# Optimization experiments

Measured on AMD Instinct MI355X. Metric: run time of the kernel, lower is better.

Reference implementation:

```python
import jax, jax.numpy as jnp
import numpy as np

KERNEL_SIZE = 4
SCALE = 0.5


def setup_inputs() -> dict:
    key = jax.random.key(0)
    k1, k2, k3 = jax.random.split(key, 3)
    M, K, N = 16384, 1024, 4096
    x = jax.random.normal(k1, (M, K), dtype=jnp.float32)
    weight = jax.random.normal(k2, (N, K), dtype=jnp.float32)
    bias = jax.random.normal(k3, (N,), dtype=jnp.float32)
    return {"x": x, "weight": weight, "bias": bias}


def reference(x, weight, bias):
    # y = x @ W^T + b : (M, N)
    y = jnp.einsum('mk,nk->mn', x, weight) + bias[None, :]
    M, N = y.shape
    valid_n = (N // KERNEL_SIZE) * KERNEL_SIZE
    # MaxPool1d(kernel_size, stride=kernel_size): (M, N//k, k) -> max over window
    pooled = jnp.max(y[:, :valid_n].reshape(M, valid_n // KERNEL_SIZE, KERNEL_SIZE), axis=-1)
    # sum over pooled features, then scale -> (M,)
    return jnp.sum(pooled, axis=-1) * SCALE
```

## Files before the change

kernel.cpp:

```cpp
#include <hip/hip_runtime.h>
#include <stdint.h>

#define M_DIM 16384
#define K_DIM 1024
#define N_DIM 4096
#define BM 128
#define BN 128
#define BK 32
#define LDSP 40

typedef __bf16 bf16;
typedef __attribute__((ext_vector_type(8))) __bf16 bf16x8;
typedef __attribute__((ext_vector_type(4))) float f32x4;

__device__ __forceinline__ uint32_t pack2_bf16(float a, float b) {
    uint32_t ua = __float_as_uint(a);
    uint32_t ub = __float_as_uint(b);
    ua += 0x7fffu + ((ua >> 16) & 1u);
    ub += 0x7fffu + ((ub >> 16) & 1u);
    return (ua >> 16) | (ub & 0xffff0000u);
}

__device__ __forceinline__ void load_lds16(const bf16* g, bf16* l) {
    __builtin_amdgcn_global_load_lds(
        (__attribute__((address_space(1))) uint32_t*)(uintptr_t)g,
        (__attribute__((address_space(3))) uint32_t*)(uintptr_t)l,
        16, 0, 0);
}

__global__ __launch_bounds__(256) void convert_bf16_kernel(
    const float* __restrict__ in, uint4* __restrict__ out, int n8)
{
    int i = blockIdx.x * blockDim.x + threadIdx.x;
    if (i >= n8) return;
    const float4* p = (const float4*)(in + (size_t)i * 8);
    float4 a = p[0], b = p[1];
    uint4 w;
    w.x = pack2_bf16(a.x, a.y);
    w.y = pack2_bf16(a.z, a.w);
    w.z = pack2_bf16(b.x, b.y);
    w.w = pack2_bf16(b.z, b.w);
    out[i] = w;
}

__global__ __launch_bounds__(256) void gemm_pool_lds_kernel(
    const bf16* __restrict__ xb, const bf16* __restrict__ wb,
    const float* __restrict__ bias, float* __restrict__ out)
{
    __shared__ bf16 sA[BM * BK];
    __shared__ bf16 sB[BN * BK];

    const int tid = threadIdx.x;
    const int bx = blockIdx.x;
    const int by = blockIdx.y;

    const int lane = tid & 63;
    const int wave = tid >> 6;
    const int wm = wave >> 1;
    const int wn = wave & 1;
    const int lr = lane & 15;
    const int quad = lane >> 4;

    const int c0row = wave * 32;
    const int grow = lane >> 2;
    const int gcol = (lane & 3) * 8;

    const bf16* Abase = xb + (size_t)(by * BM + c0row + grow) * K_DIM + gcol;
    const bf16* Bbase = wb + (size_t)(bx * BN + c0row + grow) * K_DIM + gcol;
    bf16* ldsA0 = sA + c0row * BK;
    bf16* ldsA1 = sA + (c0row + 16) * BK;
    bf16* ldsB0 = sB + c0row * BK;
    bf16* ldsB1 = sB + (c0row + 16) * BK;
    const size_t rowskip = (size_t)16 * K_DIM;

    f32x4 acc[4][4] = {};

    for (int kt = 0; kt < K_DIM; kt += BK) {
        load_lds16(Abase + kt, ldsA0);
        load_lds16(Abase + kt + rowskip, ldsA1);
        load_lds16(Bbase + kt, ldsB0);
        load_lds16(Bbase + kt + rowskip, ldsB1);
        __syncthreads();

        bf16x8 af[4], bfr[4];
        #pragma unroll
        for (int i = 0; i < 4; ++i)
            af[i] = *(const bf16x8*)(sA + (wm * 64 + i * 16 + lr) * BK + quad * 8);
        #pragma unroll
        for (int j = 0; j < 4; ++j)
            bfr[j] = *(const bf16x8*)(sB + (wn * 64 + j * 16 + lr) * BK + quad * 8);

        #pragma unroll
        for (int i = 0; i < 4; ++i)
            #pragma unroll
            for (int j = 0; j < 4; ++j)
                acc[i][j] = __builtin_amdgcn_mfma_f32_16x16x32_bf16(af[i], bfr[j], acc[i][j], 0, 0, 0);
        __syncthreads();
    }

    float bv[4];
    #pragma unroll
    for (int j = 0; j < 4; ++j)
        bv[j] = bias[bx * BN + wn * 64 + j * 16 + lr];

    #pragma unroll
    for (int i = 0; i < 4; ++i) {
        float rsum[4] = {0.f, 0.f, 0.f, 0.f};
        #pragma unroll
        for (int j = 0; j < 4; ++j) {
            #pragma unroll
            for (int r = 0; r < 4; ++r) {
                float t = acc[i][j][r] + bv[j];
                t = fmaxf(t, __shfl_xor(t, 1, 64));
                t = fmaxf(t, __shfl_xor(t, 2, 64));
                t += __shfl_xor(t, 4, 64);
                t += __shfl_xor(t, 8, 64);
                rsum[r] += t;
            }
        }
        if (lr == 0) {
            const int row = by * BM + wm * 64 + i * 16 + quad * 4;
            #pragma unroll
            for (int r = 0; r < 4; ++r)
                atomicAdd(&out[row + r], rsum[r] * 0.5f);
        }
    }
}

__global__ __launch_bounds__(256) void fused_linear_pool_kernel(
    const float* __restrict__ x, const float* __restrict__ wt,
    const float* __restrict__ bias, float* __restrict__ out)
{
    __shared__ uint32_t sA[BM * LDSP / 2];
    __shared__ uint32_t sB[BN * LDSP / 2];

    const int tid = threadIdx.x;
    const int bx = blockIdx.x;
    const int by = blockIdx.y;

    const float* Abase = x  + (size_t)by * BM * K_DIM;
    const float* Bbase = wt + (size_t)bx * BN * K_DIM;

    const int lane = tid & 63;
    const int wave = tid >> 6;
    const int wm = wave >> 1;
    const int wn = wave & 1;
    const int lr = lane & 15;
    const int quad = lane >> 4;

    const int srow  = tid >> 2;
    const int scol  = (tid & 3) * 8;
    const int swidx = (tid & 3) * 4;

    f32x4 acc[4][4] = {};

    for (int kt = 0; kt < K_DIM; kt += BK) {
        #pragma unroll
        for (int p = 0; p < 2; ++p) {
            const int r = srow + p * 64;
            const float4* ga = (const float4*)(Abase + (size_t)r * K_DIM + kt + scol);
            const float4* gb = (const float4*)(Bbase + (size_t)r * K_DIM + kt + scol);
            float4 a0 = ga[0], a1 = ga[1], b0 = gb[0], b1 = gb[1];
            uint4 wa;
            wa.x = pack2_bf16(a0.x, a0.y); wa.y = pack2_bf16(a0.z, a0.w);
            wa.z = pack2_bf16(a1.x, a1.y); wa.w = pack2_bf16(a1.z, a1.w);
            *(uint4*)&sA[r * (LDSP / 2) + swidx] = wa;
            uint4 wbv;
            wbv.x = pack2_bf16(b0.x, b0.y); wbv.y = pack2_bf16(b0.z, b0.w);
            wbv.z = pack2_bf16(b1.x, b1.y); wbv.w = pack2_bf16(b1.z, b1.w);
            *(uint4*)&sB[r * (LDSP / 2) + swidx] = wbv;
        }
        __syncthreads();

        bf16x8 af[4], bfr[4];
        #pragma unroll
        for (int i = 0; i < 4; ++i)
            af[i] = *(const bf16x8*)((const bf16*)sA + (wm * 64 + i * 16 + lr) * LDSP + quad * 8);
        #pragma unroll
        for (int j = 0; j < 4; ++j)
            bfr[j] = *(const bf16x8*)((const bf16*)sB + (wn * 64 + j * 16 + lr) * LDSP + quad * 8);

        #pragma unroll
        for (int i = 0; i < 4; ++i)
            #pragma unroll
            for (int j = 0; j < 4; ++j)
                acc[i][j] = __builtin_amdgcn_mfma_f32_16x16x32_bf16(af[i], bfr[j], acc[i][j], 0, 0, 0);
        __syncthreads();
    }

    float bv[4];
    #pragma unroll
    for (int j = 0; j < 4; ++j)
        bv[j] = bias[bx * BN + wn * 64 + j * 16 + lr];

    #pragma unroll
    for (int i = 0; i < 4; ++i) {
        float rsum[4] = {0.f, 0.f, 0.f, 0.f};
        #pragma unroll
        for (int j = 0; j < 4; ++j) {
            #pragma unroll
            for (int r = 0; r < 4; ++r) {
                float t = acc[i][j][r] + bv[j];
                t = fmaxf(t, __shfl_xor(t, 1, 64));
                t = fmaxf(t, __shfl_xor(t, 2, 64));
                t += __shfl_xor(t, 4, 64);
                t += __shfl_xor(t, 8, 64);
                rsum[r] += t;
            }
        }
        if (lr == 0) {
            const int row = by * BM + wm * 64 + i * 16 + quad * 4;
            #pragma unroll
            for (int r = 0; r < 4; ++r)
                atomicAdd(&out[row + r], rsum[r] * 0.5f);
        }
    }
}

extern "C" void kernel_launch(void* const* d_in, const int* in_sizes, int n_in,
                              void* d_out, int out_size, void* d_ws, size_t ws_size,
                              hipStream_t stream) {
    const float* x  = (const float*)d_in[0];
    const float* wt = (const float*)d_in[1];
    const float* bs = (const float*)d_in[2];
    float* out = (float*)d_out;

    hipMemsetAsync(out, 0, (size_t)out_size * sizeof(float), stream);

    const size_t xe = (size_t)M_DIM * K_DIM;
    const size_t we = (size_t)N_DIM * K_DIM;
    const size_t need = (xe + we) * sizeof(bf16);

    dim3 grid(N_DIM / BN, M_DIM / BM);

    if (ws_size >= need) {
        bf16* xb = (bf16*)d_ws;
        bf16* wb = xb + xe;
        convert_bf16_kernel<<<(int)(xe / 8 / 256), 256, 0, stream>>>(x, (uint4*)xb, (int)(xe / 8));
        convert_bf16_kernel<<<(int)(we / 8 / 256), 256, 0, stream>>>(wt, (uint4*)wb, (int)(we / 8));
        gemm_pool_lds_kernel<<<grid, 256, 0, stream>>>(xb, wb, bs, out);
    } else {
        fused_linear_pool_kernel<<<grid, 256, 0, stream>>>(x, wt, bs, out);
    }
}
```

Before: 304.1 us.

## Pre-tile and XOR-swizzle bf16 operands, double BK, merge conversion kernels

The conversion pass now writes x and W in a tiled 128x64 layout with an XOR swizzle on 16-byte chunks, and a single launch converts both tensors. The GEMM loads each contiguous tile straight into LDS and reads it back with matching swizzled addresses, which aims to remove LDS bank conflicts. BK grows from 32 to 64, halving the number of barrier pairs per K loop. The epilogue now does the cross-window sum shuffles once per row instead of once per column tile.

```diff
diff --git a/kernel.cpp b/kernel.cpp
--- a/kernel.cpp
+++ b/kernel.cpp
@@ -6,7 +6,8 @@
 #define N_DIM 4096
 #define BM 128
 #define BN 128
-#define BK 32
+#define BK 64
+#define KT_N (K_DIM / BK)
 #define LDSP 40
 
 typedef __bf16 bf16;
@@ -28,22 +29,37 @@
         16, 0, 0);
 }
 
-__global__ __launch_bounds__(256) void convert_bf16_kernel(
-    const float* __restrict__ in, uint4* __restrict__ out, int n8)
+__global__ __launch_bounds__(256) void convert_swizzle_kernel(
+    const float* __restrict__ x, const float* __restrict__ w,
+    uint4* __restrict__ xsw, uint4* __restrict__ wsw, int xchunks, int wchunks)
 {
-    int i = blockIdx.x * blockDim.x + threadIdx.x;
-    if (i >= n8) return;
-    const float4* p = (const float4*)(in + (size_t)i * 8);
+    int i = blockIdx.x * 256 + threadIdx.x;
+    const float* src;
+    uint4* dst;
+    int idx;
+    if (i < xchunks) { src = x; dst = xsw; idx = i; }
+    else             { src = w; dst = wsw; idx = i - xchunks; if (idx >= wchunks) return; }
+
+    int e = idx << 3;
+    int m = e >> 10;
+    int k = e & (K_DIM - 1);
+    int mt = m >> 7, r = m & 127;
+    int kt = k >> 6;
+    int c  = (k >> 3) & 7;
+    int tile = mt * KT_N + kt;
+    int dstoff = tile * 8192 + r * 64 + ((c ^ (r & 7)) << 3);
+
+    const float4* p = (const float4*)(src + e);
     float4 a = p[0], b = p[1];
-    uint4 w;
-    w.x = pack2_bf16(a.x, a.y);
-    w.y = pack2_bf16(a.z, a.w);
-    w.z = pack2_bf16(b.x, b.y);
-    w.w = pack2_bf16(b.z, b.w);
-    out[i] = w;
-}
-
-__global__ __launch_bounds__(256) void gemm_pool_lds_kernel(
+    uint4 out;
+    out.x = pack2_bf16(a.x, a.y);
+    out.y = pack2_bf16(a.z, a.w);
+    out.z = pack2_bf16(b.x, b.y);
+    out.w = pack2_bf16(b.z, b.w);
+    dst[dstoff >> 3] = out;
+}
+
+__global__ __launch_bounds__(256) void gemm_pool_sw_kernel(
     const bf16* __restrict__ xb, const bf16* __restrict__ wb,
     const float* __restrict__ bias, float* __restrict__ out)
 {
@@ -61,40 +77,44 @@
     const int lr = lane & 15;
     const int quad = lane >> 4;
 
-    const int c0row = wave * 32;
-    const int grow = lane >> 2;
-    const int gcol = (lane & 3) * 8;
-
-    const bf16* Abase = xb + (size_t)(by * BM + c0row + grow) * K_DIM + gcol;
-    const bf16* Bbase = wb + (size_t)(bx * BN + c0row + grow) * K_DIM + gcol;
-    bf16* ldsA0 = sA + c0row * BK;
-    bf16* ldsA1 = sA + (c0row + 16) * BK;
-    bf16* ldsB0 = sB + c0row * BK;
-    bf16* ldsB1 = sB + (c0row + 16) * BK;
-    const size_t rowskip = (size_t)16 * K_DIM;
+    const bf16* Atile0 = xb + (size_t)(by * KT_N) * 8192 + wave * 2048 + lane * 8;
+    const bf16* Btile0 = wb + (size_t)(bx * KT_N) * 8192 + wave * 2048 + lane * 8;
+    bf16* ldsA = sA + wave * 2048;
+    bf16* ldsB = sB + wave * 2048;
 
     f32x4 acc[4][4] = {};
 
-    for (int kt = 0; kt < K_DIM; kt += BK) {
-        load_lds16(Abase + kt, ldsA0);
-        load_lds16(Abase + kt + rowskip, ldsA1);
-        load_lds16(Bbase + kt, ldsB0);
-        load_lds16(Bbase + kt + rowskip, ldsB1);
-        __syncthreads();
-
-        bf16x8 af[4], bfr[4];
-        #pragma unroll
-        for (int i = 0; i < 4; ++i)
-            af[i] = *(const bf16x8*)(sA + (wm * 64 + i * 16 + lr) * BK + quad * 8);
-        #pragma unroll
-        for (int j = 0; j < 4; ++j)
-            bfr[j] = *(const bf16x8*)(sB + (wn * 64 + j * 16 + lr) * BK + quad * 8);
-
-        #pragma unroll
-        for (int i = 0; i < 4; ++i)
-            #pragma unroll
-            for (int j = 0; j < 4; ++j)
-                acc[i][j] = __builtin_amdgcn_mfma_f32_16x16x32_bf16(af[i], bfr[j], acc[i][j], 0, 0, 0);
+    for (int kt = 0; kt < KT_N; ++kt) {
+        const bf16* ga = Atile0 + kt * 8192;
+        const bf16* gb = Btile0 + kt * 8192;
+        #pragma unroll
+        for (int q = 0; q < 4; ++q) {
+            load_lds16(ga + q * 512, ldsA + q * 512);
+            load_lds16(gb + q * 512, ldsB + q * 512);
+        }
+        __syncthreads();
+
+        #pragma unroll
+        for (int s = 0; s < 2; ++s) {
+            bf16x8 af[4], bfr[4];
+            #pragma unroll
+            for (int i = 0; i < 4; ++i) {
+                int row = wm * 64 + i * 16 + lr;
+                int pos = (s * 4 + quad) ^ (row & 7);
+                af[i] = *(const bf16x8*)(sA + row * 64 + pos * 8);
+            }
+            #pragma unroll
+            for (int j = 0; j < 4; ++j) {
+                int row = wn * 64 + j * 16 + lr;
+                int pos = (s * 4 + quad) ^ (row & 7);
+                bfr[j] = *(const bf16x8*)(sB + row * 64 + pos * 8);
+            }
+            #pragma unroll
+            for (int i = 0; i < 4; ++i)
+                #pragma unroll
+                for (int j = 0; j < 4; ++j)
+                    acc[i][j] = __builtin_amdgcn_mfma_f32_16x16x32_bf16(af[i], bfr[j], acc[i][j], 0, 0, 0);
+        }
         __syncthreads();
     }
 
@@ -105,7 +125,7 @@
 
     #pragma unroll
     for (int i = 0; i < 4; ++i) {
-        float rsum[4] = {0.f, 0.f, 0.f, 0.f};
+        float rs[4] = {0.f, 0.f, 0.f, 0.f};
         #pragma unroll
         for (int j = 0; j < 4; ++j) {
             #pragma unroll
@@ -113,16 +133,19 @@
                 float t = acc[i][j][r] + bv[j];
                 t = fmaxf(t, __shfl_xor(t, 1, 64));
                 t = fmaxf(t, __shfl_xor(t, 2, 64));
-                t += __shfl_xor(t, 4, 64);
-                t += __shfl_xor(t, 8, 64);
-                rsum[r] += t;
-            }
+                rs[r] += t;
+            }
+        }
+        #pragma unroll
+        for (int r = 0; r < 4; ++r) {
+            rs[r] += __shfl_xor(rs[r], 4, 64);
+            rs[r] += __shfl_xor(rs[r], 8, 64);
         }
         if (lr == 0) {
             const int row = by * BM + wm * 64 + i * 16 + quad * 4;
             #pragma unroll
             for (int r = 0; r < 4; ++r)
-                atomicAdd(&out[row + r], rsum[r] * 0.5f);
+                atomicAdd(&out[row + r], rs[r] * 0.5f);
         }
     }
 }
@@ -154,7 +177,7 @@
 
     f32x4 acc[4][4] = {};
 
-    for (int kt = 0; kt < K_DIM; kt += BK) {
+    for (int kt = 0; kt < K_DIM; kt += 32) {
         #pragma unroll
         for (int p = 0; p < 2; ++p) {
             const int r = srow + p * 64;
@@ -236,9 +259,12 @@
     if (ws_size >= need) {
         bf16* xb = (bf16*)d_ws;
         bf16* wb = xb + xe;
-        convert_bf16_kernel<<<(int)(xe / 8 / 256), 256, 0, stream>>>(x, (uint4*)xb, (int)(xe / 8));
-        convert_bf16_kernel<<<(int)(we / 8 / 256), 256, 0, stream>>>(wt, (uint4*)wb, (int)(we / 8));
-        gemm_pool_lds_kernel<<<grid, 256, 0, stream>>>(xb, wb, bs, out);
+        const int xchunks = (int)(xe / 8);
+        const int wchunks = (int)(we / 8);
+        const int total   = xchunks + wchunks;
+        convert_swizzle_kernel<<<(total + 255) / 256, 256, 0, stream>>>(
+            x, wt, (uint4*)xb, (uint4*)wb, xchunks, wchunks);
+        gemm_pool_sw_kernel<<<grid, 256, 0, stream>>>(xb, wb, bs, out);
     } else {
         fused_linear_pool_kernel<<<grid, 256, 0, stream>>>(x, wt, bs, out);
     }
```

Measured after the change: 296.2 us. 1.03x faster.
